# Kernel optimization log

Measured on AMD Instinct MI355X. Metric: run time of the kernel, lower is better.

The kernel has to match this reference:

```python
import jax, jax.numpy as jnp
import numpy as np

B = 512          # batch of trees
L = 2048         # leaves per tree (perfect binary tree)
VOCAB = 100000
D_IN = 128       # input_dim
H = 128          # hidden_dim
NUM_CLASSES = 2


def setup_inputs() -> dict:
    key = jax.random.key(0)
    ks = jax.random.split(key, 8)
    leaf_ids = jax.random.randint(ks[0], (B, L), 0, VOCAB)
    # learned params (xavier-ish scales; exact init values don't matter for the baseline)
    embedding = jax.random.normal(ks[1], (VOCAB, D_IN), dtype=jnp.float32) * 0.1
    W_in = jax.random.normal(ks[2], (D_IN, H), dtype=jnp.float32) * (1.0 / np.sqrt(D_IN))
    b_in = jnp.zeros((H,), dtype=jnp.float32)
    W_comp = jax.random.normal(ks[3], (2 * H, H), dtype=jnp.float32) * (1.0 / np.sqrt(2 * H))
    b_comp = jnp.zeros((H,), dtype=jnp.float32)
    W_cls = jax.random.normal(ks[4], (H, NUM_CLASSES), dtype=jnp.float32) * (1.0 / np.sqrt(H))
    b_cls = jnp.zeros((NUM_CLASSES,), dtype=jnp.float32)
    return {"leaf_ids": leaf_ids, "embedding": embedding, "W_in": W_in, "b_in": b_in,
            "W_comp": W_comp, "b_comp": b_comp, "W_cls": W_cls, "b_cls": b_cls}


def reference(leaf_ids, embedding, W_in, b_in, W_comp, b_comp, W_cls, b_cls):
    # Leaves: embedding gather -> input_projection (dropout is identity in eval)
    h = embedding[leaf_ids] @ W_in + b_in            # [B, L, H]
    # Depth-batched binary composition up the perfect binary tree:
    # torch.cat([left, right]) @ composition -> tanh, level by level.
    n = L
    while n > 1:
        pairs = h.reshape(B, n // 2, 2 * H)          # contiguous (left, right) concat
        h = jnp.tanh(pairs @ W_comp + b_comp)        # [B, n//2, H]
        n //= 2
    root = h[:, 0]                                   # [B, H]
    return root @ W_cls + b_cls                      # [B, NUM_CLASSES]
```

## Files before the change

### kernel.cpp

```cpp
#include <hip/hip_runtime.h>

typedef __attribute__((ext_vector_type(8))) short s16x8;
typedef __attribute__((ext_vector_type(4))) float f32x4;

#define BB   512
#define LL   2048
#define DD   128
#define HH   128
#define SUB  128
#define NSUB (LL / SUB)
#define NBLK (BB * NSUB)
#define K1ROWS 8
#define K2ROWS (NSUB * K1ROWS)

__device__ __forceinline__ short f2bf(float x) {
  unsigned u = __builtin_bit_cast(unsigned, x);
  u += 0x7fffu + ((u >> 16) & 1u);
  return (short)(u >> 16);
}
__device__ __forceinline__ unsigned pk_bf16(float a, float b) {
  unsigned r;
  asm("v_cvt_pk_bf16_f32 %0, %1, %2" : "=v"(r) : "v"(a), "v"(b));
  return r;
}
__device__ __forceinline__ float tanh_fast(float x) {
  float e2 = __expf(2.f * x);
  return (e2 - 1.f) * __builtin_amdgcn_rcpf(e2 + 1.f);
}

__device__ __forceinline__ int swz(int row, int inner) {
  return row * 256 + (inner ^ (((row >> 1) & 7) << 4));
}

__global__ __launch_bounds__(256) void k_prep(
    const float* __restrict__ Win, const float* __restrict__ Wcomp,
    const float* __restrict__ bin, const float* __restrict__ bcomp,
    short* __restrict__ WmT, short* __restrict__ WcT,
    float* __restrict__ b1f) {
  const int b = blockIdx.x, t = threadIdx.x;
  if (b < 128) {
    const int d = b;
    const int half = t >> 7, n = t & 127;
    float acc = 0.f;
    for (int k = 0; k < 128; ++k)
      acc += Win[d * 128 + k] * Wcomp[(k + 128 * half) * 128 + n];
    WmT[n * 256 + half * 128 + d] = f2bf(acc);
  } else if (b < 160) {
    for (int idx = (b - 128) * 256 + t; idx < 128 * 256; idx += 32 * 256) {
      int n = idx >> 8, k = idx & 255;
      WcT[idx] = f2bf(Wcomp[k * 128 + n]);
    }
  } else {
    if (t < 128) {
      float acc = bcomp[t];
      for (int k = 0; k < 128; ++k)
        acc += bin[k] * (Wcomp[k * 128 + t] + Wcomp[(k + 128) * 128 + t]);
      b1f[t] = acc;
    }
  }
}

__device__ __forceinline__ void tree_mm(const short* src, int mt_in,
                                        const s16x8 (&wf)[8][2], int lm,
                                        int lh, f32x4& c0, f32x4& c1) {
  s16x8 a[8];
#pragma unroll
  for (int kt = 0; kt < 8; ++kt) {
    int k = kt * 32 + lh * 8;
    int rowbuf = 2 * (mt_in * 16 + lm) + (k >> 7);
    a[kt] = *(const s16x8*)((const char*)src + swz(rowbuf, (k & 127) * 2));
  }
  c0 = (f32x4){0.f, 0.f, 0.f, 0.f};
  c1 = (f32x4){0.f, 0.f, 0.f, 0.f};
#pragma unroll
  for (int kt = 0; kt < 8; ++kt) {
    c0 = __builtin_amdgcn_mfma_f32_16x16x32_bf16(a[kt], wf[kt][0], c0, 0, 0, 0);
    c1 = __builtin_amdgcn_mfma_f32_16x16x32_bf16(a[kt], wf[kt][1], c1, 0, 0, 0);
  }
}

__global__ __launch_bounds__(256, 3) void k_subtree(
    const int* __restrict__ ids, const float* __restrict__ emb,
    const short* __restrict__ WmT, const short* __restrict__ WcT,
    const float* __restrict__ b1f, const float* __restrict__ bcomp,
    short* __restrict__ wsbf) {
  __shared__ __align__(16) short ldsB[128 * 128];
  __shared__ __align__(16) short ldsE[64 * 128];
  const int blk = blockIdx.x, tid = threadIdx.x;
  const int wave = tid >> 6, lane = tid & 63;
  const int lh = lane >> 4, lm = lane & 15;
  const int n0 = wave * 32;
  const int col0 = n0 + 2 * lm;

  int idv[16];
#pragma unroll
  for (int it = 0; it < 16; ++it)
    idv[it] = ids[(long)blk * SUB + it * 8 + (tid >> 5)];

  const float2 b1v = *(const float2*)(b1f + col0);
  const float2 bcv = *(const float2*)(bcomp + col0);

#pragma unroll
  for (int it = 0; it < 16; ++it) {
    int r = it * 8 + (tid >> 5);
    const float4 v = ((const float4*)(emb + (long)idv[it] * DD))[tid & 31];
    uint2 pv;
    pv.x = pk_bf16(v.x, v.y);
    pv.y = pk_bf16(v.z, v.w);
    *(uint2*)((char*)ldsB + swz(r, (tid & 31) * 8)) = pv;
  }

  s16x8 wf[8][2];
#pragma unroll
  for (int kt = 0; kt < 8; ++kt)
#pragma unroll
    for (int nt = 0; nt < 2; ++nt)
      wf[kt][nt] = *(const s16x8*)(WmT + (col0 + nt) * 256 + kt * 32 + lh * 8);
  __syncthreads();

#pragma unroll 1
  for (int mt = 0; mt < 4; ++mt) {
    f32x4 c0, c1;
    tree_mm(ldsB, mt, wf, lm, lh, c0, c1);
#pragma unroll
    for (int r = 0; r < 4; ++r) {
      int row = mt * 16 + lh * 4 + r;
      *(unsigned*)((char*)ldsE + swz(row, col0 * 2)) =
          pk_bf16(tanh_fast(c0[r] + b1v.x), tanh_fast(c1[r] + b1v.y));
    }
  }

#pragma unroll
  for (int kt = 0; kt < 8; ++kt)
#pragma unroll
    for (int nt = 0; nt < 2; ++nt)
      wf[kt][nt] = *(const s16x8*)(WcT + (col0 + nt) * 256 + kt * 32 + lh * 8);
  __syncthreads();

#pragma unroll 1
  for (int mt = 0; mt < 2; ++mt) {
    f32x4 c0, c1;
    tree_mm(ldsE, mt, wf, lm, lh, c0, c1);
#pragma unroll
    for (int r = 0; r < 4; ++r) {
      int row = mt * 16 + lh * 4 + r;
      *(unsigned*)((char*)ldsB + swz(row, col0 * 2)) =
          pk_bf16(tanh_fast(c0[r] + bcv.x), tanh_fast(c1[r] + bcv.y));
    }
  }
  __syncthreads();

  {
    f32x4 c0, c1;
    tree_mm(ldsB, 0, wf, lm, lh, c0, c1);
#pragma unroll
    for (int r = 0; r < 4; ++r) {
      int row = lh * 4 + r;
      *(unsigned*)((char*)ldsE + swz(row, col0 * 2)) =
          pk_bf16(tanh_fast(c0[r] + bcv.x), tanh_fast(c1[r] + bcv.y));
    }
  }
  __syncthreads();

  {
    f32x4 c0, c1;
    tree_mm(ldsE, 0, wf, lm, lh, c0, c1);
#pragma unroll
    for (int r = 0; r < 4; ++r) {
      int row = lh * 4 + r;
      if (row < K1ROWS)
        *(unsigned*)(wsbf + ((long)blk * K1ROWS + row) * HH + col0) =
            pk_bf16(tanh_fast(c0[r] + bcv.x), tanh_fast(c1[r] + bcv.y));
    }
  }
}

__global__ __launch_bounds__(256, 2) void k_tree2(
    const short* __restrict__ wsbf, const short* __restrict__ WcT,
    const float* __restrict__ bcomp, const float* __restrict__ Wcls,
    const float* __restrict__ bcls, float* __restrict__ out) {
  __shared__ __align__(16) short srcL[128 * 128];
  __shared__ __align__(16) short dstS[64 * 128];
  __shared__ float rootL[128];
  const int b = blockIdx.x, tid = threadIdx.x;
  const int wave = tid >> 6, lane = tid & 63;
  const int lh = lane >> 4, lm = lane & 15;
  const int n0 = wave * 32;
  const int col0 = n0 + 2 * lm;

  s16x8 wfc[8][2];
#pragma unroll
  for (int kt = 0; kt < 8; ++kt)
#pragma unroll
    for (int nt = 0; nt < 2; ++nt)
      wfc[kt][nt] = *(const s16x8*)(WcT + (col0 + nt) * 256 + kt * 32 + lh * 8);
  const float2 bcv = *(const float2*)(bcomp + col0);

#pragma unroll
  for (int it = 0; it < 8; ++it) {
    int row = it * 16 + (tid >> 4);
    s16x8 v = *(const s16x8*)(wsbf + ((long)b * K2ROWS + row) * HH + (tid & 15) * 8);
    *(s16x8*)((char*)srcL + swz(row, (tid & 15) * 16)) = v;
  }
  __syncthreads();

  const short* src = srcL;
  short* dst = dstS;
  const int mtiles[7] = {4, 2, 1, 1, 1, 1, 1};
  const int rlim[7] = {64, 32, 16, 8, 4, 2, 1};
#pragma unroll 1
  for (int lev = 0; lev < 7; ++lev) {
    int nmt = mtiles[lev], rl = rlim[lev];
#pragma unroll 1
    for (int mt = 0; mt < nmt; ++mt) {
      f32x4 c0, c1;
      tree_mm(src, mt, wfc, lm, lh, c0, c1);
      if (lev == 6) {
        if (lh == 0) {
          rootL[col0] = tanh_fast(c0[0] + bcv.x);
          rootL[col0 + 1] = tanh_fast(c1[0] + bcv.y);
        }
      } else {
#pragma unroll
        for (int r = 0; r < 4; ++r) {
          int row = mt * 16 + lh * 4 + r;
          if (row < rl)
            *(unsigned*)((char*)dst + swz(row, col0 * 2)) =
                pk_bf16(tanh_fast(c0[r] + bcv.x), tanh_fast(c1[r] + bcv.y));
        }
      }
    }
    __syncthreads();
    const short* t = src;
    src = dst;
    dst = (short*)t;
  }

  if (wave == 0) {
    int c = lane & 1, kb = lane >> 1;
    float p = 0.f;
#pragma unroll
    for (int j = 0; j < 4; ++j) {
      int k = kb + 32 * j;
      p += rootL[k] * Wcls[k * 2 + c];
    }
#pragma unroll
    for (int m = 2; m <= 32; m <<= 1) p += __shfl_xor(p, m, 64);
    if (lane < 2) out[b * 2 + lane] = p + bcls[lane];
  }
}

extern "C" void kernel_launch(void* const* d_in, const int* in_sizes, int n_in,
                              void* d_out, int out_size, void* d_ws, size_t ws_size,
                              hipStream_t stream) {
  const int*   ids   = (const int*)d_in[0];
  const float* emb   = (const float*)d_in[1];
  const float* Win   = (const float*)d_in[2];
  const float* bin   = (const float*)d_in[3];
  const float* Wcomp = (const float*)d_in[4];
  const float* bcomp = (const float*)d_in[5];
  const float* Wcls  = (const float*)d_in[6];
  const float* bcls  = (const float*)d_in[7];
  char* wsb = (char*)d_ws;
  short* wsbf = (short*)wsb;
  const size_t WSBF_BYTES = (size_t)BB * NSUB * K1ROWS * HH * 2;
  short* WcT = (short*)(wsb + WSBF_BYTES);
  short* WmT = (short*)(wsb + WSBF_BYTES + (64 << 10));
  float* b1f = (float*)(wsb + WSBF_BYTES + (192 << 10));
  float* out = (float*)d_out;

  hipLaunchKernelGGL(k_prep, dim3(161), dim3(256), 0, stream,
                     Win, Wcomp, bin, bcomp, WmT, WcT, b1f);
  hipLaunchKernelGGL(k_subtree, dim3(NBLK), dim3(256), 0, stream,
                     ids, emb, WmT, WcT, b1f, bcomp, wsbf);
  hipLaunchKernelGGL(k_tree2, dim3(BB), dim3(256), 0, stream,
                     wsbf, WcT, bcomp, Wcls, bcls, out);
}
```

Baseline: 175.7 us.

## Pipeline embedding gathers with leaf projection MFMA tiles in subtree kernel

The kernel now loads only the first 32 embedding rows before the first sync. The remaining rows are gathered in chunks that are issued before each leaf-projection MFMA tile and written to LDS afterwards, so gather latency overlaps with compute. The composition weights are loaded in the last iteration, and a barrier now sits in every iteration. This costs extra registers and more syncs, which may lower occupancy under launch_bounds(256,3).

Result: no change. 177.4 us (+1.0%).

```diff
diff --git a/kernel.cpp b/kernel.cpp
--- a/kernel.cpp
+++ b/kernel.cpp
@@ -91,23 +91,24 @@
   const int lh = lane >> 4, lm = lane & 15;
   const int n0 = wave * 32;
   const int col0 = n0 + 2 * lm;
+  const int gr = tid >> 5;
+  const int gc = tid & 31;
 
   int idv[16];
 #pragma unroll
   for (int it = 0; it < 16; ++it)
-    idv[it] = ids[(long)blk * SUB + it * 8 + (tid >> 5)];
+    idv[it] = ids[(long)blk * SUB + it * 8 + gr];
 
   const float2 b1v = *(const float2*)(b1f + col0);
   const float2 bcv = *(const float2*)(bcomp + col0);
 
 #pragma unroll
-  for (int it = 0; it < 16; ++it) {
-    int r = it * 8 + (tid >> 5);
-    const float4 v = ((const float4*)(emb + (long)idv[it] * DD))[tid & 31];
+  for (int it = 0; it < 4; ++it) {
+    const float4 v = ((const float4*)(emb + (long)idv[it] * DD))[gc];
     uint2 pv;
     pv.x = pk_bf16(v.x, v.y);
     pv.y = pk_bf16(v.z, v.w);
-    *(uint2*)((char*)ldsB + swz(r, (tid & 31) * 8)) = pv;
+    *(uint2*)((char*)ldsB + swz(it * 8 + gr, gc * 8)) = pv;
   }
 
   s16x8 wf[8][2];
@@ -118,8 +119,14 @@
       wf[kt][nt] = *(const s16x8*)(WmT + (col0 + nt) * 256 + kt * 32 + lh * 8);
   __syncthreads();
 
-#pragma unroll 1
+#pragma unroll
   for (int mt = 0; mt < 4; ++mt) {
+    float4 g[4];
+    if (mt < 3) {
+#pragma unroll
+      for (int j = 0; j < 4; ++j)
+        g[j] = ((const float4*)(emb + (long)idv[(mt + 1) * 4 + j] * DD))[gc];
+    }
     f32x4 c0, c1;
     tree_mm(ldsB, mt, wf, lm, lh, c0, c1);
 #pragma unroll
@@ -128,14 +135,25 @@
       *(unsigned*)((char*)ldsE + swz(row, col0 * 2)) =
           pk_bf16(tanh_fast(c0[r] + b1v.x), tanh_fast(c1[r] + b1v.y));
     }
-  }
-
-#pragma unroll
-  for (int kt = 0; kt < 8; ++kt)
-#pragma unroll
-    for (int nt = 0; nt < 2; ++nt)
-      wf[kt][nt] = *(const s16x8*)(WcT + (col0 + nt) * 256 + kt * 32 + lh * 8);
-  __syncthreads();
+    if (mt < 3) {
+#pragma unroll
+      for (int j = 0; j < 4; ++j) {
+        int it = (mt + 1) * 4 + j;
+        uint2 pv;
+        pv.x = pk_bf16(g[j].x, g[j].y);
+        pv.y = pk_bf16(g[j].z, g[j].w);
+        *(uint2*)((char*)ldsB + swz(it * 8 + gr, gc * 8)) = pv;
+      }
+    } else {
+#pragma unroll
+      for (int kt = 0; kt < 8; ++kt)
+#pragma unroll
+        for (int nt = 0; nt < 2; ++nt)
+          wf[kt][nt] =
+              *(const s16x8*)(WcT + (col0 + nt) * 256 + kt * 32 + lh * 8);
+    }
+    __syncthreads();
+  }
 
 #pragma unroll 1
   for (int mt = 0; mt < 2; ++mt) {
```

## Split subtree kernel columns across 8 waves with one MFMA tile each

Applied to the files above, without the earlier changes.

The subtree kernel moves from 4 waves each computing two 16-column MFMA tiles to 8 waves (512 threads) each computing one 16-column tile. Per-thread weight registers are halved and the launch bound now asks for 6 blocks of 512 threads. The aim is more waves in flight per CU to hide gather latency from the embedding lookup. In exchange, each wave reloads the shared A fragments for fewer MFMAs, and outputs are written as scalar bf16 stores instead of packed pairs, which raises LDS and global store instruction counts.

New measurement: 175.7 us. Within noise of the previous version (+0.0%).

```diff
diff --git a/kernel.cpp b/kernel.cpp
--- a/kernel.cpp
+++ b/kernel.cpp
@@ -60,9 +60,9 @@
   }
 }
 
-__device__ __forceinline__ void tree_mm(const short* src, int mt_in,
-                                        const s16x8 (&wf)[8][2], int lm,
-                                        int lh, f32x4& c0, f32x4& c1) {
+__device__ __forceinline__ f32x4 tree_mm1(const short* src, int mt_in,
+                                          const s16x8 (&wf)[8], int lm,
+                                          int lh) {
   s16x8 a[8];
 #pragma unroll
   for (int kt = 0; kt < 8; ++kt) {
@@ -70,16 +70,14 @@
     int rowbuf = 2 * (mt_in * 16 + lm) + (k >> 7);
     a[kt] = *(const s16x8*)((const char*)src + swz(rowbuf, (k & 127) * 2));
   }
-  c0 = (f32x4){0.f, 0.f, 0.f, 0.f};
-  c1 = (f32x4){0.f, 0.f, 0.f, 0.f};
-#pragma unroll
-  for (int kt = 0; kt < 8; ++kt) {
-    c0 = __builtin_amdgcn_mfma_f32_16x16x32_bf16(a[kt], wf[kt][0], c0, 0, 0, 0);
-    c1 = __builtin_amdgcn_mfma_f32_16x16x32_bf16(a[kt], wf[kt][1], c1, 0, 0, 0);
-  }
-}
-
-__global__ __launch_bounds__(256, 3) void k_subtree(
+  f32x4 c = {0.f, 0.f, 0.f, 0.f};
+#pragma unroll
+  for (int kt = 0; kt < 8; ++kt)
+    c = __builtin_amdgcn_mfma_f32_16x16x32_bf16(a[kt], wf[kt], c, 0, 0, 0);
+  return c;
+}
+
+__global__ __launch_bounds__(512, 6) void k_subtree(
     const int* __restrict__ ids, const float* __restrict__ emb,
     const short* __restrict__ WmT, const short* __restrict__ WcT,
     const float* __restrict__ b1f, const float* __restrict__ bcomp,
@@ -89,88 +87,77 @@
   const int blk = blockIdx.x, tid = threadIdx.x;
   const int wave = tid >> 6, lane = tid & 63;
   const int lh = lane >> 4, lm = lane & 15;
-  const int n0 = wave * 32;
-  const int col0 = n0 + 2 * lm;
-
-  int idv[16];
-#pragma unroll
-  for (int it = 0; it < 16; ++it)
-    idv[it] = ids[(long)blk * SUB + it * 8 + (tid >> 5)];
-
-  const float2 b1v = *(const float2*)(b1f + col0);
-  const float2 bcv = *(const float2*)(bcomp + col0);
-
-#pragma unroll
-  for (int it = 0; it < 16; ++it) {
-    int r = it * 8 + (tid >> 5);
-    const float4 v = ((const float4*)(emb + (long)idv[it] * DD))[tid & 31];
+  const int col0 = wave * 16 + lm;
+  const int gr = tid >> 5;
+  const int gc = tid & 31;
+
+  int idv[8];
+#pragma unroll
+  for (int it = 0; it < 8; ++it)
+    idv[it] = ids[(long)blk * SUB + it * 16 + gr];
+
+  const float b1s = b1f[col0];
+  const float bcs = bcomp[col0];
+
+#pragma unroll
+  for (int it = 0; it < 8; ++it) {
+    int r = it * 16 + gr;
+    const float4 v = ((const float4*)(emb + (long)idv[it] * DD))[gc];
     uint2 pv;
     pv.x = pk_bf16(v.x, v.y);
     pv.y = pk_bf16(v.z, v.w);
-    *(uint2*)((char*)ldsB + swz(r, (tid & 31) * 8)) = pv;
-  }
-
-  s16x8 wf[8][2];
-#pragma unroll
-  for (int kt = 0; kt < 8; ++kt)
-#pragma unroll
-    for (int nt = 0; nt < 2; ++nt)
-      wf[kt][nt] = *(const s16x8*)(WmT + (col0 + nt) * 256 + kt * 32 + lh * 8);
+    *(uint2*)((char*)ldsB + swz(r, gc * 8)) = pv;
+  }
+
+  s16x8 wf[8];
+#pragma unroll
+  for (int kt = 0; kt < 8; ++kt)
+    wf[kt] = *(const s16x8*)(WmT + col0 * 256 + kt * 32 + lh * 8);
   __syncthreads();
 
 #pragma unroll 1
   for (int mt = 0; mt < 4; ++mt) {
-    f32x4 c0, c1;
-    tree_mm(ldsB, mt, wf, lm, lh, c0, c1);
+    f32x4 c = tree_mm1(ldsB, mt, wf, lm, lh);
 #pragma unroll
     for (int r = 0; r < 4; ++r) {
       int row = mt * 16 + lh * 4 + r;
-      *(unsigned*)((char*)ldsE + swz(row, col0 * 2)) =
-          pk_bf16(tanh_fast(c0[r] + b1v.x), tanh_fast(c1[r] + b1v.y));
-    }
-  }
-
-#pragma unroll
-  for (int kt = 0; kt < 8; ++kt)
-#pragma unroll
-    for (int nt = 0; nt < 2; ++nt)
-      wf[kt][nt] = *(const s16x8*)(WcT + (col0 + nt) * 256 + kt * 32 + lh * 8);
+      *(short*)((char*)ldsE + swz(row, col0 * 2)) = f2bf(tanh_fast(c[r] + b1s));
+    }
+  }
+#pragma unroll
+  for (int kt = 0; kt < 8; ++kt)
+    wf[kt] = *(const s16x8*)(WcT + col0 * 256 + kt * 32 + lh * 8);
   __syncthreads();
 
 #pragma unroll 1
   for (int mt = 0; mt < 2; ++mt) {
-    f32x4 c0, c1;
-    tree_mm(ldsE, mt, wf, lm, lh, c0, c1);
+    f32x4 c = tree_mm1(ldsE, mt, wf, lm, lh);
 #pragma unroll
     for (int r = 0; r < 4; ++r) {
       int row = mt * 16 + lh * 4 + r;
-      *(unsigned*)((char*)ldsB + swz(row, col0 * 2)) =
-          pk_bf16(tanh_fast(c0[r] + bcv.x), tanh_fast(c1[r] + bcv.y));
+      *(short*)((char*)ldsB + swz(row, col0 * 2)) = f2bf(tanh_fast(c[r] + bcs));
     }
   }
   __syncthreads();
 
   {
-    f32x4 c0, c1;
-    tree_mm(ldsB, 0, wf, lm, lh, c0, c1);
+    f32x4 c = tree_mm1(ldsB, 0, wf, lm, lh);
 #pragma unroll
     for (int r = 0; r < 4; ++r) {
       int row = lh * 4 + r;
-      *(unsigned*)((char*)ldsE + swz(row, col0 * 2)) =
-          pk_bf16(tanh_fast(c0[r] + bcv.x), tanh_fast(c1[r] + bcv.y));
+      *(short*)((char*)ldsE + swz(row, col0 * 2)) = f2bf(tanh_fast(c[r] + bcs));
     }
   }
   __syncthreads();
 
   {
-    f32x4 c0, c1;
-    tree_mm(ldsE, 0, wf, lm, lh, c0, c1);
+    f32x4 c = tree_mm1(ldsE, 0, wf, lm, lh);
 #pragma unroll
     for (int r = 0; r < 4; ++r) {
       int row = lh * 4 + r;
       if (row < K1ROWS)
-        *(unsigned*)(wsbf + ((long)blk * K1ROWS + row) * HH + col0) =
-            pk_bf16(tanh_fast(c0[r] + bcv.x), tanh_fast(c1[r] + bcv.y));
+        wsbf[((long)blk * K1ROWS + row) * HH + col0] =
+            f2bf(tanh_fast(c[r] + bcs));
     }
   }
 }
@@ -213,8 +200,19 @@
     int nmt = mtiles[lev], rl = rlim[lev];
 #pragma unroll 1
     for (int mt = 0; mt < nmt; ++mt) {
-      f32x4 c0, c1;
-      tree_mm(src, mt, wfc, lm, lh, c0, c1);
+      s16x8 a[8];
+#pragma unroll
+      for (int kt = 0; kt < 8; ++kt) {
+        int k = kt * 32 + lh * 8;
+        int rowbuf = 2 * (mt * 16 + lm) + (k >> 7);
+        a[kt] = *(const s16x8*)((const char*)src + swz(rowbuf, (k & 127) * 2));
+      }
+      f32x4 c0 = {0.f, 0.f, 0.f, 0.f}, c1 = {0.f, 0.f, 0.f, 0.f};
+#pragma unroll
+      for (int kt = 0; kt < 8; ++kt) {
+        c0 = __builtin_amdgcn_mfma_f32_16x16x32_bf16(a[kt], wfc[kt][0], c0, 0, 0, 0);
+        c1 = __builtin_amdgcn_mfma_f32_16x16x32_bf16(a[kt], wfc[kt][1], c1, 0, 0, 0);
+      }
       if (lev == 6) {
         if (lh == 0) {
           rootL[col0] = tanh_fast(c0[0] + bcv.x);
@@ -271,7 +269,7 @@
 
   hipLaunchKernelGGL(k_prep, dim3(161), dim3(256), 0, stream,
                      Win, Wcomp, bin, bcomp, WmT, WcT, b1f);
-  hipLaunchKernelGGL(k_subtree, dim3(NBLK), dim3(256), 0, stream,
+  hipLaunchKernelGGL(k_subtree, dim3(NBLK), dim3(512), 0, stream,
                      ids, emb, WmT, WcT, b1f, bcomp, wsbf);
   hipLaunchKernelGGL(k_tree2, dim3(BB), dim3(256), 0, stream,
                      wsbf, WcT, bcomp, Wcls, bcls, out);
```
